# Optimization experiments

Hardware: AMD Instinct MI355X
Metric: run time of the kernel (lower is better)

Reference implementation:

```python
import jax, jax.numpy as jnp
import numpy as np

N = 50000          # nodes
E = 800000         # directed edges (before self-loops)
IN_C = 512
HID = 256
HEADS = 8
HEAD_C = HID // HEADS
OUT_C = 64
NEG_SLOPE = 0.2    # PyG GATConv default LeakyReLU slope
EPS = 1e-16        # PyG softmax denominator epsilon


def _gat_layer(h, src, dst, a_src, a_dst):
    """One GATConv propagate step (eval mode, no attention dropout).
    h: [N, H, C] transformed node features; src/dst: [Etot] edge endpoints.
    Returns aggregated [N, H, C]."""
    # per-node attention logits: [N, H]
    alpha_src = jnp.einsum('nhc,hc->nh', h, a_src)
    alpha_dst = jnp.einsum('nhc,hc->nh', h, a_dst)
    e = alpha_src[src] + alpha_dst[dst]                      # [Etot, H]
    e = jnp.where(e > 0, e, NEG_SLOPE * e)                   # LeakyReLU
    # segment softmax over incoming edges of each dst node
    e_max = jax.ops.segment_max(e, dst, num_segments=N)      # [N, H]
    e_exp = jnp.exp(e - e_max[dst])                          # [Etot, H]
    denom = jax.ops.segment_sum(e_exp, dst, num_segments=N)  # [N, H]
    alpha = e_exp / (denom[dst] + EPS)                       # [Etot, H]
    msg = alpha[:, :, None] * h[src]                         # [Etot, H, C]
    return jax.ops.segment_sum(msg, dst, num_segments=N)     # [N, H, C]


def setup_inputs() -> dict:
    key = jax.random.key(0)
    ks = jax.random.split(key, 10)
    s1 = 1.0 / np.sqrt(IN_C)
    s2 = 1.0 / np.sqrt(HID)
    return {
        'x': jax.random.normal(ks[0], (N, IN_C), jnp.float32),
        'edge_index': jax.random.randint(ks[1], (2, E), 0, N, dtype=jnp.int64),
        'W1': jax.random.normal(ks[2], (IN_C, HID), jnp.float32) * s1,
        'a_src1': jax.random.normal(ks[3], (HEADS, HEAD_C), jnp.float32) * 0.1,
        'a_dst1': jax.random.normal(ks[4], (HEADS, HEAD_C), jnp.float32) * 0.1,
        'b1': jnp.zeros((HID,), jnp.float32),
        'W2': jax.random.normal(ks[5], (HID, OUT_C), jnp.float32) * s2,
        'a_src2': jax.random.normal(ks[6], (1, OUT_C), jnp.float32) * 0.1,
        'a_dst2': jax.random.normal(ks[7], (1, OUT_C), jnp.float32) * 0.1,
        'b2': jnp.zeros((OUT_C,), jnp.float32),
    }


def reference(x, edge_index, W1, a_src1, a_dst1, b1, W2, a_src2, a_dst2, b2):
    # PyG GATConv: add self-loops (default add_self_loops=True)
    loops = jnp.arange(N, dtype=edge_index.dtype)
    src = jnp.concatenate([edge_index[0], loops])
    dst = jnp.concatenate([edge_index[1], loops])

    # conv1: heads=8, concat=True
    h1 = (x @ W1).reshape(N, HEADS, HEAD_C)
    h1 = _gat_layer(h1, src, dst, a_src1, a_dst1).reshape(N, HID) + b1
    h1 = jax.nn.elu(h1)

    # conv2: heads=1, concat=False (mean over 1 head == identity)
    h2 = (h1 @ W2).reshape(N, 1, OUT_C)
    out = _gat_layer(h2, src, dst, a_src2, a_dst2).mean(axis=1) + b2
    return out
```

## Files before the change

kernel.cpp:

```cpp
#include <hip/hip_runtime.h>

#define N_NODES 50000
#define M_PAD   50048
#define NBLK    196
#define E_EDGES 800000
#define E_TOT   (E_EDGES + N_NODES)
#define IN_C 512
#define HID 256
#define HEADS 8
#define OUT_C 64

#define MM1_BX 391
#define MM1_BLK (MM1_BX * 2)
#define SCAT_BLOCKS ((E_TOT + 255) / 256)
#define CNT_BLOCKS  ((E_TOT + 511) / 512)
#define CONVW_ELEMS (HID * IN_C + OUT_C * HID)
#define CONVW_BLOCKS ((CONVW_ELEMS + 511) / 512)

typedef unsigned int uint;
typedef unsigned short ushort_t;
typedef __bf16 bf16x8 __attribute__((ext_vector_type(8)));
typedef float f32x4 __attribute__((ext_vector_type(4)));
typedef float f32x2 __attribute__((ext_vector_type(2)));

__device__ __forceinline__ float lrelu(float x) { return x > 0.f ? x : 0.2f * x; }

__device__ __forceinline__ unsigned short f2bf(float f) {
  __bf16 b = (__bf16)f;
  return __builtin_bit_cast(unsigned short, b);
}
__device__ __forceinline__ float bflo(uint u) { return __uint_as_float(u << 16); }
__device__ __forceinline__ float bfhi(uint u) { return __uint_as_float(u & 0xFFFF0000u); }
__device__ __forceinline__ f32x2 unp2(uint u) {
  f32x2 r; r.x = bflo(u); r.y = bfhi(u); return r;
}

__global__ __launch_bounds__(512) void k_fatA(const int* __restrict__ ei,
                                              int* __restrict__ counts,
                                              const float* __restrict__ W1,
                                              const float* __restrict__ W2,
                                              ushort_t* __restrict__ w1t,
                                              ushort_t* __restrict__ w2t) {
  int bid = blockIdx.x;
  if (bid < CNT_BLOCKS) {
    int e = bid * 512 + threadIdx.x;
    if (e >= E_TOT) return;
    int d = (e < E_EDGES) ? ei[E_EDGES + e] : (e - E_EDGES);
    atomicAdd(&counts[d], 1);
  } else {
    int t = (bid - CNT_BLOCKS) * 512 + threadIdx.x;
    if (t < HID * IN_C) {
      int n = t >> 9, k = t & 511;
      w1t[t] = f2bf(W1[(size_t)k * HID + n]);
    } else if (t < CONVW_ELEMS) {
      int u = t - HID * IN_C;
      int n = u >> 8, k = u & 255;
      w2t[u] = f2bf(W2[(size_t)k * OUT_C + n]);
    }
  }
}

__global__ void k_bsum(const int* __restrict__ counts, int* __restrict__ bsum) {
  int i = blockIdx.x * 256 + threadIdx.x;
  int v = (i < N_NODES) ? counts[i] : 0;
  __shared__ int ws[4];
  int lane = threadIdx.x & 63, wid = threadIdx.x >> 6;
  #pragma unroll
  for (int off = 32; off; off >>= 1) v += __shfl_xor(v, off);
  if (lane == 0) ws[wid] = v;
  __syncthreads();
  if (threadIdx.x == 0) bsum[blockIdx.x] = ws[0] + ws[1] + ws[2] + ws[3];
}

__global__ void k_bscan(const int* __restrict__ bsum, int* __restrict__ boff) {
  int tid = threadIdx.x;
  int v = (tid < NBLK) ? bsum[tid] : 0;
  int lane = tid & 63, wid = tid >> 6;
  int x = v;
  #pragma unroll
  for (int off = 1; off < 64; off <<= 1) {
    int t = __shfl_up(x, off);
    if (lane >= off) x += t;
  }
  __shared__ int ws[4];
  if (lane == 63) ws[wid] = x;
  __syncthreads();
  int woff = 0;
  for (int w = 0; w < wid; w++) woff += ws[w];
  if (tid < NBLK) boff[tid] = x + woff - v;
}

__global__ void k_local(const int* __restrict__ counts, const int* __restrict__ boff,
                        int* __restrict__ indptr, int* __restrict__ wptr) {
  int b = blockIdx.x;
  int i = b * 256 + threadIdx.x;
  int v = (i < N_NODES) ? counts[i] : 0;
  int lane = threadIdx.x & 63, wid = threadIdx.x >> 6;
  int x = v;
  #pragma unroll
  for (int off = 1; off < 64; off <<= 1) {
    int t = __shfl_up(x, off);
    if (lane >= off) x += t;
  }
  __shared__ int ws[4];
  if (lane == 63) ws[wid] = x;
  __syncthreads();
  int woff = boff[b];
  for (int w = 0; w < wid; w++) woff += ws[w];
  int excl = woff + x - v;
  if (i < N_NODES) { indptr[i] = excl; wptr[i] = excl; }
  if (b == 0 && threadIdx.x == 0) indptr[N_NODES] = E_TOT;
}

__global__ __launch_bounds__(256) void k_fatB(const float* __restrict__ A,
                                              const ushort_t* __restrict__ Bt,
                                              const float* __restrict__ asrc1,
                                              const float* __restrict__ adst1,
                                              ushort_t* __restrict__ Cb,
                                              float* __restrict__ as1,
                                              float* __restrict__ ad1,
                                              const int* __restrict__ ei,
                                              int* __restrict__ wptr,
                                              int* __restrict__ csr_src) {
  if (blockIdx.x >= MM1_BLK) {
    int e = (blockIdx.x - MM1_BLK) * 256 + threadIdx.x;
    if (e >= E_TOT) return;
    int s, d;
    if (e < E_EDGES) { s = ei[e]; d = ei[E_EDGES + e]; }
    else { s = d = e - E_EDGES; }
    int pos = atomicAdd(&wptr[d], 1);
    csr_src[pos] = s;
    return;
  }
  int bx = blockIdx.x >> 1, by = blockIdx.x & 1;
  __shared__ ushort_t sA[128][40];
  __shared__ ushort_t sB[128][40];
  int tid = threadIdx.x;
  int wid = tid >> 6, lane = tid & 63;
  int wm = wid >> 1, wn = wid & 1;
  int lr = lane & 15, kg = lane >> 4;
  int row0 = bx * 128;
  int cb0 = by * 128;
  f32x4 acc[4][4] = {};

  for (int k0 = 0; k0 < IN_C; k0 += 32) {
    {
      int r = tid >> 1, cs = (tid & 1) * 16;
      int gr = row0 + r;
      unsigned short v[16];
      if (gr < N_NODES) {
        const float* src = A + (size_t)gr * IN_C + k0 + cs;
        #pragma unroll
        for (int i = 0; i < 4; i++) {
          float4 f = *reinterpret_cast<const float4*>(src + i * 4);
          v[i * 4 + 0] = f2bf(f.x); v[i * 4 + 1] = f2bf(f.y);
          v[i * 4 + 2] = f2bf(f.z); v[i * 4 + 3] = f2bf(f.w);
        }
      } else {
        #pragma unroll
        for (int i = 0; i < 16; i++) v[i] = 0;
      }
      uint4 p0, p1;
      p0.x = v[0] | ((uint)v[1] << 16);  p0.y = v[2] | ((uint)v[3] << 16);
      p0.z = v[4] | ((uint)v[5] << 16);  p0.w = v[6] | ((uint)v[7] << 16);
      p1.x = v[8] | ((uint)v[9] << 16);  p1.y = v[10] | ((uint)v[11] << 16);
      p1.z = v[12] | ((uint)v[13] << 16); p1.w = v[14] | ((uint)v[15] << 16);
      *reinterpret_cast<uint4*>(&sA[r][cs]) = p0;
      *reinterpret_cast<uint4*>(&sA[r][cs + 8]) = p1;
    }
    {
      int n = tid >> 1, ks = (tid & 1) * 16;
      const ushort_t* src = Bt + (size_t)(cb0 + n) * IN_C + k0 + ks;
      uint4 v0 = *reinterpret_cast<const uint4*>(src);
      uint4 v1 = *reinterpret_cast<const uint4*>(src + 8);
      *reinterpret_cast<uint4*>(&sB[n][ks]) = v0;
      *reinterpret_cast<uint4*>(&sB[n][ks + 8]) = v1;
    }
    __syncthreads();

    bf16x8 af[4], bfr[4];
    #pragma unroll
    for (int i = 0; i < 4; i++)
      af[i] = *reinterpret_cast<const bf16x8*>(&sA[wm * 64 + i * 16 + lr][kg * 8]);
    #pragma unroll
    for (int j = 0; j < 4; j++)
      bfr[j] = *reinterpret_cast<const bf16x8*>(&sB[wn * 64 + j * 16 + lr][kg * 8]);
    #pragma unroll
    for (int i = 0; i < 4; i++)
      #pragma unroll
      for (int j = 0; j < 4; j++)
        acc[i][j] = __builtin_amdgcn_mfma_f32_16x16x32_bf16(af[i], bfr[j], acc[i][j], 0, 0, 0);
    __syncthreads();
  }

  {
    int h0 = by * 4 + wn * 2, h1 = h0 + 1;
    float a0s = asrc1[h0 * 32 + lr], a1s = asrc1[h0 * 32 + 16 + lr];
    float a2s = asrc1[h1 * 32 + lr], a3s = asrc1[h1 * 32 + 16 + lr];
    float a0d = adst1[h0 * 32 + lr], a1d = adst1[h0 * 32 + 16 + lr];
    float a2d = adst1[h1 * 32 + lr], a3d = adst1[h1 * 32 + 16 + lr];
    #pragma unroll
    for (int i = 0; i < 4; i++) {
      #pragma unroll
      for (int q = 0; q < 4; q++) {
        float s0 = acc[i][0][q] * a0s + acc[i][1][q] * a1s;
        float s1 = acc[i][2][q] * a2s + acc[i][3][q] * a3s;
        float d0 = acc[i][0][q] * a0d + acc[i][1][q] * a1d;
        float d1 = acc[i][2][q] * a2d + acc[i][3][q] * a3d;
        #pragma unroll
        for (int off = 1; off < 16; off <<= 1) {
          s0 += __shfl_xor(s0, off);
          s1 += __shfl_xor(s1, off);
          d0 += __shfl_xor(d0, off);
          d1 += __shfl_xor(d1, off);
        }
        int gr = row0 + wm * 64 + i * 16 + kg * 4 + q;
        if (lr == 0 && gr < N_NODES) {
          as1[gr * 8 + h0] = s0;
          as1[gr * 8 + h1] = s1;
          ad1[gr * 8 + h0] = d0;
          ad1[gr * 8 + h1] = d1;
        }
      }
    }
  }

  #pragma unroll
  for (int i = 0; i < 4; i++) {
    #pragma unroll
    for (int j = 0; j < 4; j++) {
      int gc = cb0 + wn * 64 + j * 16 + lr;
      #pragma unroll
      for (int q = 0; q < 4; q++) {
        int gr = row0 + wm * 64 + i * 16 + kg * 4 + q;
        if (gr < N_NODES) Cb[(size_t)gr * HID + gc] = f2bf(acc[i][j][q]);
      }
    }
  }
}

__global__ __launch_bounds__(256) void k_mm2(const ushort_t* __restrict__ At,
                                             const ushort_t* __restrict__ Bt,
                                             const float* __restrict__ asrc2,
                                             const float* __restrict__ adst2,
                                             ushort_t* __restrict__ Cb,
                                             float* __restrict__ as2,
                                             float* __restrict__ ad2) {
  __shared__ ushort_t sA[128][40];
  __shared__ ushort_t sB[64][40];
  int tid = threadIdx.x;
  int wid = tid >> 6, lane = tid & 63;
  int lr = lane & 15, kg = lane >> 4;
  int row0 = blockIdx.x * 128;
  f32x4 acc[2][4] = {};

  for (int kt = 0; kt < HID / 32; ++kt) {
    {
      const ushort_t* src = At + ((size_t)blockIdx.x * 8 + kt) * 4096 + tid * 16;
      uint4 v0 = *reinterpret_cast<const uint4*>(src);
      uint4 v1 = *reinterpret_cast<const uint4*>(src + 8);
      int r = tid >> 1, ks = (tid & 1) * 16;
      *reinterpret_cast<uint4*>(&sA[r][ks]) = v0;
      *reinterpret_cast<uint4*>(&sA[r][ks + 8]) = v1;
    }
    if (tid < 128) {
      int n = tid >> 1, ks = (tid & 1) * 16;
      const ushort_t* src = Bt + (size_t)n * HID + kt * 32 + ks;
      uint4 v0 = *reinterpret_cast<const uint4*>(src);
      uint4 v1 = *reinterpret_cast<const uint4*>(src + 8);
      *reinterpret_cast<uint4*>(&sB[n][ks]) = v0;
      *reinterpret_cast<uint4*>(&sB[n][ks + 8]) = v1;
    }
    __syncthreads();

    bf16x8 af[2], bfr[4];
    #pragma unroll
    for (int i = 0; i < 2; i++)
      af[i] = *reinterpret_cast<const bf16x8*>(&sA[wid * 32 + i * 16 + lr][kg * 8]);
    #pragma unroll
    for (int j = 0; j < 4; j++)
      bfr[j] = *reinterpret_cast<const bf16x8*>(&sB[j * 16 + lr][kg * 8]);
    #pragma unroll
    for (int i = 0; i < 2; i++)
      #pragma unroll
      for (int j = 0; j < 4; j++)
        acc[i][j] = __builtin_amdgcn_mfma_f32_16x16x32_bf16(af[i], bfr[j], acc[i][j], 0, 0, 0);
    __syncthreads();
  }

  {
    float avs[4], avd[4];
    #pragma unroll
    for (int j = 0; j < 4; j++) {
      avs[j] = asrc2[j * 16 + lr];
      avd[j] = adst2[j * 16 + lr];
    }
    #pragma unroll
    for (int i = 0; i < 2; i++) {
      #pragma unroll
      for (int q = 0; q < 4; q++) {
        float s = acc[i][0][q] * avs[0] + acc[i][1][q] * avs[1]
                + acc[i][2][q] * avs[2] + acc[i][3][q] * avs[3];
        float d = acc[i][0][q] * avd[0] + acc[i][1][q] * avd[1]
                + acc[i][2][q] * avd[2] + acc[i][3][q] * avd[3];
        #pragma unroll
        for (int off = 1; off < 16; off <<= 1) {
          s += __shfl_xor(s, off);
          d += __shfl_xor(d, off);
        }
        int gr = row0 + wid * 32 + i * 16 + kg * 4 + q;
        if (lr == 0 && gr < N_NODES) { as2[gr] = s; ad2[gr] = d; }
      }
    }
  }

  #pragma unroll
  for (int i = 0; i < 2; i++) {
    #pragma unroll
    for (int j = 0; j < 4; j++) {
      int gc = j * 16 + lr;
      #pragma unroll
      for (int q = 0; q < 4; q++) {
        int gr = row0 + wid * 32 + i * 16 + kg * 4 + q;
        if (gr < N_NODES) Cb[(size_t)gr * OUT_C + gc] = f2bf(acc[i][j][q]);
      }
    }
  }
}

__global__ __launch_bounds__(256) void k_agg1(const ushort_t* __restrict__ h1b,
                                              const int* __restrict__ indptr,
                                              const int* __restrict__ csr_src,
                                              const float* __restrict__ as1,
                                              const float* __restrict__ ad1,
                                              const float* __restrict__ b1,
                                              ushort_t* __restrict__ hpb) {
  int wave = threadIdx.x >> 6, lane = threadIdx.x & 63;
  int node = blockIdx.x * 4 + wave;
  if (node >= N_NODES) return;
  int beg = indptr[node], end = indptr[node + 1];
  int half = lane >> 5, sl = lane & 31, h = sl >> 2;
  float adst = ad1[node * 8 + h];

  f32x2 a0 = {0.f, 0.f}, a1 = {0.f, 0.f}, a2 = {0.f, 0.f}, a3 = {0.f, 0.f};
  float dsum = 0.f;
  int e = beg + half;
  for (; e + 6 < end; e += 8) {
    int s0 = csr_src[e];
    int s1 = csr_src[e + 2];
    int s2 = csr_src[e + 4];
    int s3 = csr_src[e + 6];
    float l0 = as1[s0 * 8 + h];
    float l1 = as1[s1 * 8 + h];
    float l2 = as1[s2 * 8 + h];
    float l3 = as1[s3 * 8 + h];
    uint4 r0 = *reinterpret_cast<const uint4*>(&h1b[(size_t)s0 * HID + sl * 8]);
    uint4 r1 = *reinterpret_cast<const uint4*>(&h1b[(size_t)s1 * HID + sl * 8]);
    uint4 r2 = *reinterpret_cast<const uint4*>(&h1b[(size_t)s2 * HID + sl * 8]);
    uint4 r3 = *reinterpret_cast<const uint4*>(&h1b[(size_t)s3 * HID + sl * 8]);
    float w0 = __expf(lrelu(l0 + adst));
    float w1 = __expf(lrelu(l1 + adst));
    float w2 = __expf(lrelu(l2 + adst));
    float w3 = __expf(lrelu(l3 + adst));
    a0 += w0 * unp2(r0.x); a1 += w0 * unp2(r0.y); a2 += w0 * unp2(r0.z); a3 += w0 * unp2(r0.w);
    a0 += w1 * unp2(r1.x); a1 += w1 * unp2(r1.y); a2 += w1 * unp2(r1.z); a3 += w1 * unp2(r1.w);
    a0 += w2 * unp2(r2.x); a1 += w2 * unp2(r2.y); a2 += w2 * unp2(r2.z); a3 += w2 * unp2(r2.w);
    a0 += w3 * unp2(r3.x); a1 += w3 * unp2(r3.y); a2 += w3 * unp2(r3.z); a3 += w3 * unp2(r3.w);
    dsum += w0 + w1 + w2 + w3;
  }
  for (; e < end; e += 2) {
    int s = csr_src[e];
    float w = __expf(lrelu(as1[s * 8 + h] + adst));
    uint4 rv = *reinterpret_cast<const uint4*>(&h1b[(size_t)s * HID + sl * 8]);
    a0 += w * unp2(rv.x); a1 += w * unp2(rv.y); a2 += w * unp2(rv.z); a3 += w * unp2(rv.w);
    dsum += w;
  }
  float acc[8] = {a0.x, a0.y, a1.x, a1.y, a2.x, a2.y, a3.x, a3.y};
  #pragma unroll
  for (int j = 0; j < 8; j++) acc[j] += __shfl_xor(acc[j], 32);
  dsum += __shfl_xor(dsum, 32);
  float inv = 1.f / (dsum + 1e-16f);

  if (half == 0) {
    unsigned short ob[8];
    #pragma unroll
    for (int j = 0; j < 8; j++) {
      float o = acc[j] * inv + b1[sl * 8 + j];
      o = o > 0.f ? o : expm1f(o);
      ob[j] = f2bf(o);
    }
    uint4 pk;
    pk.x = ob[0] | ((uint)ob[1] << 16); pk.y = ob[2] | ((uint)ob[3] << 16);
    pk.z = ob[4] | ((uint)ob[5] << 16); pk.w = ob[6] | ((uint)ob[7] << 16);
    size_t addr = ((size_t)(node >> 7) * 8 + (sl >> 2)) * 4096 + (size_t)(node & 127) * 32 + (sl & 3) * 8;
    *reinterpret_cast<uint4*>(&hpb[addr]) = pk;
  }
}

__global__ __launch_bounds__(256) void k_agg2(const ushort_t* __restrict__ h2b,
                                              const int* __restrict__ indptr,
                                              const int* __restrict__ csr_src,
                                              const float* __restrict__ as2,
                                              const float* __restrict__ ad2,
                                              const float* __restrict__ b2,
                                              float* __restrict__ out) {
  int wave = threadIdx.x >> 6, lane = threadIdx.x & 63;
  int node = blockIdx.x * 4 + wave;
  if (node >= N_NODES) return;
  int beg = indptr[node], end = indptr[node + 1];
  int half = lane >> 5, sl = lane & 31;
  float adst = ad2[node];

  f32x2 acc2 = {0.f, 0.f};
  float dsum = 0.f;
  int e = beg + half;
  for (; e + 6 < end; e += 8) {
    int s0 = csr_src[e];
    int s1 = csr_src[e + 2];
    int s2 = csr_src[e + 4];
    int s3 = csr_src[e + 6];
    float l0 = as2[s0];
    float l1 = as2[s1];
    float l2 = as2[s2];
    float l3 = as2[s3];
    uint v0 = *reinterpret_cast<const uint*>(&h2b[(size_t)s0 * OUT_C + sl * 2]);
    uint v1 = *reinterpret_cast<const uint*>(&h2b[(size_t)s1 * OUT_C + sl * 2]);
    uint v2 = *reinterpret_cast<const uint*>(&h2b[(size_t)s2 * OUT_C + sl * 2]);
    uint v3 = *reinterpret_cast<const uint*>(&h2b[(size_t)s3 * OUT_C + sl * 2]);
    float w0 = __expf(lrelu(l0 + adst));
    float w1 = __expf(lrelu(l1 + adst));
    float w2 = __expf(lrelu(l2 + adst));
    float w3 = __expf(lrelu(l3 + adst));
    acc2 += w0 * unp2(v0); acc2 += w1 * unp2(v1);
    acc2 += w2 * unp2(v2); acc2 += w3 * unp2(v3);
    dsum += w0 + w1 + w2 + w3;
  }
  for (; e < end; e += 2) {
    int s = csr_src[e];
    float w = __expf(lrelu(as2[s] + adst));
    uint v = *reinterpret_cast<const uint*>(&h2b[(size_t)s * OUT_C + sl * 2]);
    acc2 += w * unp2(v);
    dsum += w;
  }
  acc2.x += __shfl_xor(acc2.x, 32);
  acc2.y += __shfl_xor(acc2.y, 32);
  dsum += __shfl_xor(dsum, 32);
  float inv = 1.f / (dsum + 1e-16f);
  if (half == 0) {
    float2 o = {acc2.x * inv + b2[sl * 2], acc2.y * inv + b2[sl * 2 + 1]};
    *reinterpret_cast<float2*>(&out[(size_t)node * OUT_C + sl * 2]) = o;
  }
}

extern "C" void kernel_launch(void* const* d_in, const int* in_sizes, int n_in,
                              void* d_out, int out_size, void* d_ws, size_t ws_size,
                              hipStream_t stream) {
  const float* x     = (const float*)d_in[0];
  const int*   ei    = (const int*)d_in[1];
  const float* W1    = (const float*)d_in[2];
  const float* asrc1 = (const float*)d_in[3];
  const float* adst1 = (const float*)d_in[4];
  const float* b1    = (const float*)d_in[5];
  const float* W2    = (const float*)d_in[6];
  const float* asrc2 = (const float*)d_in[7];
  const float* adst2 = (const float*)d_in[8];
  const float* b2    = (const float*)d_in[9];
  float* out = (float*)d_out;

  char* p = (char*)d_ws;
  size_t off = 0;
  auto take = [&](size_t bytes) -> void* {
    void* r = p + off;
    off += (bytes + 255) & ~(size_t)255;
    return r;
  };
  ushort_t* h1b  = (ushort_t*)take((size_t)N_NODES * HID * 2);
  ushort_t* hpb  = (ushort_t*)take((size_t)(M_PAD / 128) * 8 * 4096 * 2);
  ushort_t* h2b  = (ushort_t*)take((size_t)N_NODES * OUT_C * 2);
  float*    as1  = (float*)take((size_t)N_NODES * HEADS * 4);
  float*    ad1  = (float*)take((size_t)N_NODES * HEADS * 4);
  float*    as2  = (float*)take((size_t)N_NODES * 4);
  float*    ad2  = (float*)take((size_t)N_NODES * 4);
  int* counts = (int*)take((size_t)N_NODES * 4);
  int* indptr = (int*)take((size_t)(N_NODES + 1) * 4);
  int* wptr   = (int*)take((size_t)(N_NODES + 1) * 4);
  int* bsum   = (int*)take((size_t)NBLK * 4);
  int* boff   = (int*)take((size_t)NBLK * 4);
  int* csr    = (int*)take((size_t)E_TOT * 4);
  ushort_t* w1t = (ushort_t*)take((size_t)IN_C * HID * 2);
  ushort_t* w2t = (ushort_t*)take((size_t)HID * OUT_C * 2);

  hipMemsetAsync(counts, 0, (size_t)N_NODES * 4, stream);
  k_fatA<<<CNT_BLOCKS + CONVW_BLOCKS, 512, 0, stream>>>(ei, counts, W1, W2, w1t, w2t);
  k_bsum<<<NBLK, 256, 0, stream>>>(counts, bsum);
  k_bscan<<<1, 256, 0, stream>>>(bsum, boff);
  k_local<<<NBLK, 256, 0, stream>>>(counts, boff, indptr, wptr);

  k_fatB<<<MM1_BLK + SCAT_BLOCKS, 256, 0, stream>>>(x, w1t, asrc1, adst1, h1b, as1, ad1,
                                                    ei, wptr, csr);

  k_agg1<<<(N_NODES + 3) / 4, 256, 0, stream>>>(h1b, indptr, csr, as1, ad1, b1, hpb);

  k_mm2<<<M_PAD / 128, 256, 0, stream>>>(hpb, w2t, asrc2, adst2, h2b, as2, ad2);
  k_agg2<<<(N_NODES + 3) / 4, 256, 0, stream>>>(h2b, indptr, csr, as2, ad2, b2, out);
}
```

Baseline: 238.7 us.

## Double-buffer LDS tiles and prefetch next K-slice in first GEMM

The first GEMM's main loop now uses two LDS buffers for A and B. The global loads for the next K tile go into registers before the MFMAs on the current tile run, and they are written to the other buffer afterward. This hides global-load latency behind compute and drops one barrier per iteration. In exchange it doubles LDS use for these tiles and raises register pressure, which may lower occupancy.

```diff
diff --git a/kernel.cpp b/kernel.cpp
--- a/kernel.cpp
+++ b/kernel.cpp
@@ -133,8 +133,8 @@
     return;
   }
   int bx = blockIdx.x >> 1, by = blockIdx.x & 1;
-  __shared__ ushort_t sA[128][40];
-  __shared__ ushort_t sB[128][40];
+  __shared__ ushort_t sA[2][128][40];
+  __shared__ ushort_t sB[2][128][40];
   int tid = threadIdx.x;
   int wid = tid >> 6, lane = tid & 63;
   int wm = wid >> 1, wn = wid & 1;
@@ -143,54 +143,68 @@
   int cb0 = by * 128;
   f32x4 acc[4][4] = {};
 
-  for (int k0 = 0; k0 < IN_C; k0 += 32) {
-    {
-      int r = tid >> 1, cs = (tid & 1) * 16;
-      int gr = row0 + r;
-      unsigned short v[16];
-      if (gr < N_NODES) {
-        const float* src = A + (size_t)gr * IN_C + k0 + cs;
-        #pragma unroll
-        for (int i = 0; i < 4; i++) {
-          float4 f = *reinterpret_cast<const float4*>(src + i * 4);
-          v[i * 4 + 0] = f2bf(f.x); v[i * 4 + 1] = f2bf(f.y);
-          v[i * 4 + 2] = f2bf(f.z); v[i * 4 + 3] = f2bf(f.w);
-        }
-      } else {
-        #pragma unroll
-        for (int i = 0; i < 16; i++) v[i] = 0;
-      }
-      uint4 p0, p1;
-      p0.x = v[0] | ((uint)v[1] << 16);  p0.y = v[2] | ((uint)v[3] << 16);
-      p0.z = v[4] | ((uint)v[5] << 16);  p0.w = v[6] | ((uint)v[7] << 16);
-      p1.x = v[8] | ((uint)v[9] << 16);  p1.y = v[10] | ((uint)v[11] << 16);
-      p1.z = v[12] | ((uint)v[13] << 16); p1.w = v[14] | ((uint)v[15] << 16);
-      *reinterpret_cast<uint4*>(&sA[r][cs]) = p0;
-      *reinterpret_cast<uint4*>(&sA[r][cs + 8]) = p1;
-    }
-    {
-      int n = tid >> 1, ks = (tid & 1) * 16;
-      const ushort_t* src = Bt + (size_t)(cb0 + n) * IN_C + k0 + ks;
-      uint4 v0 = *reinterpret_cast<const uint4*>(src);
-      uint4 v1 = *reinterpret_cast<const uint4*>(src + 8);
-      *reinterpret_cast<uint4*>(&sB[n][ks]) = v0;
-      *reinterpret_cast<uint4*>(&sB[n][ks + 8]) = v1;
-    }
-    __syncthreads();
-
+  int ar = tid >> 1, acs = (tid & 1) * 16;
+  int garow = row0 + ar;
+  bool avalid = garow < N_NODES;
+  const float* aptr = A + (size_t)(avalid ? garow : 0) * IN_C + acs;
+  const ushort_t* bptr = Bt + (size_t)(cb0 + ar) * IN_C + acs;
+
+  float4 fa0, fa1, fa2, fa3;
+  uint4 bv0, bv1;
+
+  auto loadAB = [&](int k0) {
+    if (avalid) {
+      fa0 = *reinterpret_cast<const float4*>(aptr + k0);
+      fa1 = *reinterpret_cast<const float4*>(aptr + k0 + 4);
+      fa2 = *reinterpret_cast<const float4*>(aptr + k0 + 8);
+      fa3 = *reinterpret_cast<const float4*>(aptr + k0 + 12);
+    } else {
+      fa0 = make_float4(0.f, 0.f, 0.f, 0.f);
+      fa1 = fa0; fa2 = fa0; fa3 = fa0;
+    }
+    bv0 = *reinterpret_cast<const uint4*>(bptr + k0);
+    bv1 = *reinterpret_cast<const uint4*>(bptr + k0 + 8);
+  };
+  auto writeAB = [&](int buf) {
+    unsigned short v[16];
+    v[0] = f2bf(fa0.x);  v[1] = f2bf(fa0.y);  v[2] = f2bf(fa0.z);  v[3] = f2bf(fa0.w);
+    v[4] = f2bf(fa1.x);  v[5] = f2bf(fa1.y);  v[6] = f2bf(fa1.z);  v[7] = f2bf(fa1.w);
+    v[8] = f2bf(fa2.x);  v[9] = f2bf(fa2.y);  v[10] = f2bf(fa2.z); v[11] = f2bf(fa2.w);
+    v[12] = f2bf(fa3.x); v[13] = f2bf(fa3.y); v[14] = f2bf(fa3.z); v[15] = f2bf(fa3.w);
+    uint4 p0, p1;
+    p0.x = v[0] | ((uint)v[1] << 16);  p0.y = v[2] | ((uint)v[3] << 16);
+    p0.z = v[4] | ((uint)v[5] << 16);  p0.w = v[6] | ((uint)v[7] << 16);
+    p1.x = v[8] | ((uint)v[9] << 16);  p1.y = v[10] | ((uint)v[11] << 16);
+    p1.z = v[12] | ((uint)v[13] << 16); p1.w = v[14] | ((uint)v[15] << 16);
+    *reinterpret_cast<uint4*>(&sA[buf][ar][acs]) = p0;
+    *reinterpret_cast<uint4*>(&sA[buf][ar][acs + 8]) = p1;
+    *reinterpret_cast<uint4*>(&sB[buf][ar][acs]) = bv0;
+    *reinterpret_cast<uint4*>(&sB[buf][ar][acs + 8]) = bv1;
+  };
+
+  loadAB(0);
+  writeAB(0);
+  __syncthreads();
+  int cur = 0;
+  for (int kt = 0; kt < IN_C / 32; ++kt) {
+    if (kt + 1 < IN_C / 32) loadAB((kt + 1) * 32);
     bf16x8 af[4], bfr[4];
     #pragma unroll
     for (int i = 0; i < 4; i++)
-      af[i] = *reinterpret_cast<const bf16x8*>(&sA[wm * 64 + i * 16 + lr][kg * 8]);
+      af[i] = *reinterpret_cast<const bf16x8*>(&sA[cur][wm * 64 + i * 16 + lr][kg * 8]);
     #pragma unroll
     for (int j = 0; j < 4; j++)
-      bfr[j] = *reinterpret_cast<const bf16x8*>(&sB[wn * 64 + j * 16 + lr][kg * 8]);
+      bfr[j] = *reinterpret_cast<const bf16x8*>(&sB[cur][wn * 64 + j * 16 + lr][kg * 8]);
     #pragma unroll
     for (int i = 0; i < 4; i++)
       #pragma unroll
       for (int j = 0; j < 4; j++)
         acc[i][j] = __builtin_amdgcn_mfma_f32_16x16x32_bf16(af[i], bfr[j], acc[i][j], 0, 0, 0);
-    __syncthreads();
+    if (kt + 1 < IN_C / 32) {
+      writeAB(cur ^ 1);
+      __syncthreads();
+      cur ^= 1;
+    }
   }
 
   {
```

Result: no change. 241.4 us (+1.1%).
